# Performance work log

Measured on AMD Instinct MI355X. Metric: run time of the kernel, lower is better.

The kernel has to match this reference:

```python
import jax, jax.numpy as jnp
import numpy as np

B, L, DIM = 4, 2048, 256
NSETS, PP, POSP, LTMP = 4, 4, 16, 16
PI = float(np.pi)


def setup_inputs() -> dict:
    key = jax.random.key(0)
    ks = jax.random.split(key, 8)
    d = DIM
    return {
        "x": jax.random.normal(ks[0], (B, L, d), jnp.float32),
        "key_proj": jax.random.normal(ks[1], (d, NSETS * PP), jnp.float32) / np.sqrt(d),
        "query_proj": jax.random.normal(ks[2], (d, NSETS * PP), jnp.float32) / np.sqrt(d),
        "ltm_key_proj": jax.random.normal(ks[3], (3 * d, LTMP), jnp.float32) / np.sqrt(3 * d),
        "pos_freqs": jnp.exp(jnp.arange(POSP, dtype=jnp.float32) * (-np.log(10000.0) / POSP)),
        "w_value": jax.random.normal(ks[4], (d, d), jnp.float32) / np.sqrt(d),
        "b_value": jnp.zeros(d, jnp.float32),
        "w_ltm_val": jax.random.normal(ks[5], (d, d), jnp.float32) / np.sqrt(d),
        "b_ltm_val": jnp.zeros(d, jnp.float32),
        "ln_gamma": jnp.ones(d, jnp.float32),
        "ln_beta": jnp.zeros(d, jnp.float32),
        "w_out": jax.random.normal(ks[6], (d, d), jnp.float32) / np.sqrt(d),
        "b_out": jnp.zeros(d, jnp.float32),
        "set_weights": jnp.ones(NSETS, jnp.float32),
        "pos_weight": jnp.ones(1, jnp.float32),
        "surprise_scale": jnp.array(5.0, jnp.float32),
        "surprise_bias": jnp.array(0.0, jnp.float32),
        "resonance_scale": jnp.array(5.0, jnp.float32),
        "resonance_threshold": jnp.array(0.3, jnp.float32),
        "ltm_weight": jnp.array(0.5, jnp.float32),
        "ltm_binding_memory": jnp.zeros((LTMP, d), jnp.complex64),
        "ltm_count": jnp.array(0.0, jnp.float32),
    }


def reference(x, key_proj, query_proj, ltm_key_proj, pos_freqs, w_value, b_value,
              w_ltm_val, b_ltm_val, ln_gamma, ln_beta, w_out, b_out, set_weights,
              pos_weight, surprise_scale, surprise_bias, resonance_scale,
              resonance_threshold, ltm_weight, ltm_binding_memory, ltm_count):
    Bx, Lx, D = x.shape
    # phasor encodings
    key_ph = jnp.exp(1j * (jnp.tanh(x @ key_proj) * PI)).reshape(Bx, Lx, NSETS, PP)
    qry_ph = jnp.exp(1j * (jnp.tanh(x @ query_proj) * PI)).reshape(Bx, Lx, NSETS, PP)
    V_real = x @ w_value + b_value
    weights = jax.nn.softmax(set_weights)
    # joint (cross-bank) phasors
    jk = jnp.prod(key_ph, axis=2)   # [B,L,PP]
    jq = jnp.prod(qry_ph, axis=2)
    # exclusive cumsum of joint keys -> resonance-based surprise write gate
    km = jnp.concatenate([jnp.zeros_like(jk[:, :1]), jnp.cumsum(jk[:, :-1], axis=1)], axis=1)
    rmag = jnp.abs(km * jnp.conj(jq)).mean(-1, keepdims=True)
    posf = jnp.maximum(jnp.arange(Lx, dtype=jnp.float32), 1.0)
    nres = rmag / jnp.sqrt(posf)[None, :, None]
    sc = jnp.clip(resonance_scale, 1.0, 20.0)
    th = jnp.clip(resonance_threshold, 0.1, 0.9)
    surprise = 0.5 * (1.0 - jnp.tanh(sc * (nres - th)))
    gate = jax.nn.sigmoid(surprise_scale * (surprise - 0.5) + surprise_bias)
    Vg = (V_real * gate).astype(jnp.complex64)
    # cross-bank holographic memory (joint key binding)
    cross = jnp.real((jnp.cumsum(jk[..., None] * Vg[:, :, None, :], axis=1)
                      * jnp.conj(jq)[..., None]).sum(2))
    # per-bank holographic memory over all planes
    bound_all = key_ph[..., None] * Vg[:, :, None, None, :]            # [B,L,S,P,D]
    mem_all = jnp.cumsum(bound_all.reshape(Bx, Lx, NSETS * PP, D), axis=1)
    mem_all = mem_all.reshape(Bx, Lx, NSETS, PP, D)
    per_bank = jnp.real((mem_all * jnp.conj(qry_ph)[..., None]).sum(3))  # [B,L,S,D]
    total = (per_bank * weights[None, None, :, None]).sum(2)
    total = (total + cross) / (NSETS + 1.0)
    # positional phasor memory (ungated V)
    pos_ph = jnp.exp(1j * (jnp.arange(Lx, dtype=jnp.float32)[:, None] * pos_freqs * 2.0 * PI))  # [L,P]
    Vc = V_real.astype(jnp.complex64)
    ret_pos = jnp.real((jnp.cumsum(pos_ph[None, :, :, None] * Vc[:, :, None, :], axis=1)
                        * jnp.conj(pos_ph)[None, :, :, None]).sum(2))
    total = 0.5 * total + 0.5 * (jax.nn.sigmoid(pos_weight) * ret_pos)  # fixed_gate = 0.5
    # LTM retrieval from persistent binding memory (detached buffers)
    p1 = jnp.arange(1, Lx + 1, dtype=jnp.float32)[None, :, None]
    rm = jnp.cumsum(x, axis=1) / p1
    rv = jnp.cumsum(x * x, axis=1) / p1 - rm * rm
    rs = jnp.sqrt(jnp.clip(rv, 1e-8, None))
    ltm_ph = jnp.exp(1j * (jnp.tanh(jnp.concatenate([x, rm, rs], -1) @ ltm_key_proj) * PI))  # [B,L,LTMP]
    pers = jnp.real((ltm_binding_memory[None, None] * jnp.conj(ltm_ph)[..., None]).sum(2))
    pnorm = jnp.sqrt(jnp.maximum(ltm_count, 1.0) * LTMP)
    total = total + jax.nn.sigmoid(ltm_weight) * (pers / pnorm)
    # output: LayerNorm + Linear on normalized retrieval, residual
    nrm = jnp.sqrt(jnp.arange(1, Lx + 1, dtype=jnp.float32) * PP)[None, :, None]
    h = total / nrm
    mu = h.mean(-1, keepdims=True)
    var = ((h - mu) ** 2).mean(-1, keepdims=True)
    hn = (h - mu) / jnp.sqrt(var + 1e-5) * ln_gamma + ln_beta
    return x + hn @ w_out + b_out
```

## Files before the change

kernel.cpp:

```cpp
#include <hip/hip_runtime.h>
#include <math.h>

#define B 4
#define L 2048
#define D 256
#define POSP 16
#define LTMP 16
#define T 64
#define C 32
#define F 72
#define PI_F 3.14159274101257324f
#define TWO_PI_D 6.283185307179586476925286766559

__global__ __launch_bounds__(256) void prep_kernel(const float* __restrict__ pos_freqs,
                                                   const float* __restrict__ lkp,
                                                   const float* __restrict__ x,
                                                   float* __restrict__ posci,
                                                   float* __restrict__ Wt,
                                                   float* __restrict__ Sx16,
                                                   float* __restrict__ Sxx16) {
    int bid = blockIdx.x;
    int tid = threadIdx.x;
    if (bid < 128) {
        int idx = bid * 256 + tid;
        int t = idx >> 4, p = idx & 15;
        float a = (float)t * pos_freqs[p];
        float th = (a * 2.0f) * PI_F;
        double r = fmod((double)th, TWO_PI_D);
        posci[t * 32 + 2 * p] = (float)cos(r);
        posci[t * 32 + 2 * p + 1] = (float)sin(r);
    } else if (bid < 176) {
        int i2 = (bid - 128) * 256 + tid;
        if (i2 < 16 * 768) {
            int p = i2 / 768, j = i2 - p * 768;
            Wt[i2] = lkp[j * 16 + p];
        }
    } else {
        int sb = bid - 176;
        int s = sb & 127, b = sb >> 7;
        float sx = 0.f, sxx = 0.f;
#pragma unroll
        for (int k = 0; k < 16; k++) {
            float v = x[((size_t)(b * L + s * 16 + k)) * D + tid];
            sx += v; sxx += v * v;
        }
        Sx16[((size_t)(b * 128 + s)) * D + tid] = sx;
        Sxx16[((size_t)(b * 128 + s)) * D + tid] = sxx;
    }
}

__global__ __launch_bounds__(256) void featurize_kernel(
    const float* __restrict__ x, const float* __restrict__ key_proj,
    const float* __restrict__ query_proj, const float* __restrict__ w_value,
    const float* __restrict__ b_value, const float* __restrict__ set_weights,
    float* __restrict__ V, float* __restrict__ fk, float* __restrict__ fq,
    float* __restrict__ partial) {
    int cg = blockIdx.x;
    int rc = blockIdx.y;
    int b  = blockIdx.z;
    int row0 = rc * 64;
    int tid = threadIdx.x;
    __shared__ float xs[2][32][74];
    __shared__ float ws[2][32][84];
    __shared__ float zbuf[64][20];
    __shared__ float jkv[64][9];
    const bool has_proj = (cg < 2);
    const float* proj = (cg == 0) ? key_proj : query_proj;
    int rg = tid >> 4, cgi = tid & 15;
    int r0 = rg * 4, c0 = cgi * 4;
    int prow = tid >> 2, pc4 = tid & 3;
    float acc[4][4], accp[4];
#pragma unroll
    for (int i = 0; i < 4; i++) {
#pragma unroll
        for (int e = 0; e < 4; e++) acc[i][e] = 0.f;
        accp[i] = 0.f;
    }
    int rrA = tid >> 3, k4A = tid & 7;
    int jA = tid >> 4, c4A = tid & 15;
    float4 xr0, xr1, wr0, wr1, prr;

#define ISSUE_LOADS(kb_)                                                            \
    {                                                                               \
        xr0 = *(const float4*)(x + ((size_t)(b * L + row0 + rrA)) * D + (kb_) + k4A * 4);      \
        xr1 = *(const float4*)(x + ((size_t)(b * L + row0 + 32 + rrA)) * D + (kb_) + k4A * 4); \
        wr0 = *(const float4*)(w_value + (size_t)((kb_) + jA) * D + cg * 64 + c4A * 4);        \
        wr1 = *(const float4*)(w_value + (size_t)((kb_) + 16 + jA) * D + cg * 64 + c4A * 4);   \
        if (has_proj && tid < 128)                                                  \
            prr = *(const float4*)(proj + (size_t)((kb_) + (tid >> 2)) * 16 + (tid & 3) * 4);  \
    }
#define WRITE_LDS(bi)                                                               \
    {                                                                               \
        const float* xp0 = (const float*)&xr0;                                      \
        const float* xp1 = (const float*)&xr1;                                      \
        _Pragma("unroll")                                                           \
        for (int u = 0; u < 4; u++) {                                               \
            xs[bi][k4A * 4 + u][rrA] = xp0[u];                                      \
            xs[bi][k4A * 4 + u][32 + rrA] = xp1[u];                                 \
        }                                                                           \
        *(float4*)&ws[bi][jA][c4A * 4] = wr0;                                       \
        *(float4*)&ws[bi][16 + jA][c4A * 4] = wr1;                                  \
        if (has_proj && tid < 128)                                                  \
            *(float4*)&ws[bi][tid >> 2][64 + (tid & 3) * 4] = prr;                  \
    }

    ISSUE_LOADS(0);
    WRITE_LDS(0);
    __syncthreads();
    for (int kc = 0; kc < 8; kc++) {
        if (kc < 7) ISSUE_LOADS((kc + 1) * 32);
        int bi = kc & 1;
#pragma unroll 8
        for (int j = 0; j < 32; j++) {
            float2 xlo = *(float2*)&xs[bi][j][r0];
            float2 xhi = *(float2*)&xs[bi][j][r0 + 2];
            float4 wv = *(float4*)&ws[bi][j][c0];
            acc[0][0] += xlo.x * wv.x; acc[0][1] += xlo.x * wv.y; acc[0][2] += xlo.x * wv.z; acc[0][3] += xlo.x * wv.w;
            acc[1][0] += xlo.y * wv.x; acc[1][1] += xlo.y * wv.y; acc[1][2] += xlo.y * wv.z; acc[1][3] += xlo.y * wv.w;
            acc[2][0] += xhi.x * wv.x; acc[2][1] += xhi.x * wv.y; acc[2][2] += xhi.x * wv.z; acc[2][3] += xhi.x * wv.w;
            acc[3][0] += xhi.y * wv.x; acc[3][1] += xhi.y * wv.y; acc[3][2] += xhi.y * wv.z; acc[3][3] += xhi.y * wv.w;
            if (has_proj) {
                float xp = xs[bi][j][prow];
                float4 wp = *(float4*)&ws[bi][j][64 + pc4 * 4];
                accp[0] += xp * wp.x; accp[1] += xp * wp.y;
                accp[2] += xp * wp.z; accp[3] += xp * wp.w;
            }
        }
        if (kc < 7) WRITE_LDS((kc + 1) & 1);
        __syncthreads();
    }
#undef ISSUE_LOADS
#undef WRITE_LDS

    {
        int d0 = cg * 64 + c0;
        float4 bv = *(const float4*)(b_value + d0);
#pragma unroll
        for (int i = 0; i < 4; i++) {
            size_t o = ((size_t)(b * L + row0 + r0 + i)) * D + d0;
            *(float4*)(V + o) = make_float4(acc[i][0] + bv.x, acc[i][1] + bv.y,
                                            acc[i][2] + bv.z, acc[i][3] + bv.w);
        }
    }
    if (!has_proj) return;
#pragma unroll
    for (int e = 0; e < 4; e++) zbuf[prow][pc4 * 4 + e] = tanhf(accp[e]) * PI_F;
    __syncthreads();
    {
        int tt = tid >> 2, q = tid & 3;
        size_t bt = (size_t)(b * L + row0 + tt);
        if (cg == 0) {
            float* fp = fk + bt * 40;
#pragma unroll
            for (int e = 0; e < 4; e++) {
                int col = q * 4 + e;
                float si, co; sincosf(zbuf[tt][col], &si, &co);
                fp[2 * col] = co; fp[2 * col + 1] = si;
            }
            float zs = zbuf[tt][q] + zbuf[tt][4 + q] + zbuf[tt][8 + q] + zbuf[tt][12 + q];
            float si, co; sincosf(zs, &si, &co);
            fp[32 + 2 * q] = co; fp[33 + 2 * q] = si;
            jkv[tt][2 * q] = co; jkv[tt][2 * q + 1] = si;
        } else {
            float sw0 = set_weights[0], sw1 = set_weights[1], sw2 = set_weights[2], sw3 = set_weights[3];
            float mx = fmaxf(fmaxf(sw0, sw1), fmaxf(sw2, sw3));
            float e0 = expf(sw0 - mx), e1 = expf(sw1 - mx), e2 = expf(sw2 - mx), e3 = expf(sw3 - mx);
            float esum = e0 + e1 + e2 + e3;
            float wsoft[4] = {e0 / esum, e1 / esum, e2 / esum, e3 / esum};
            float* fp = fq + bt * 40;
#pragma unroll
            for (int e = 0; e < 4; e++) {
                int col = q * 4 + e;
                float si, co; sincosf(zbuf[tt][col], &si, &co);
                float sc = 0.1f * wsoft[col >> 2];
                fp[2 * col] = sc * co; fp[2 * col + 1] = sc * si;
            }
            float zs = zbuf[tt][q] + zbuf[tt][4 + q] + zbuf[tt][8 + q] + zbuf[tt][12 + q];
            float si, co; sincosf(zs, &si, &co);
            fp[32 + 2 * q] = 0.1f * co; fp[33 + 2 * q] = 0.1f * si;
        }
    }
    __syncthreads();
    if (cg == 0) {
        int h = tid >> 7, idxr = tid & 127;
        int rr2 = idxr >> 3, ch = idxr & 7;
#pragma unroll
        for (int s2 = 16; s2 >= 1; s2 >>= 1) {
            if (rr2 < s2) jkv[h * 32 + rr2][ch] += jkv[h * 32 + rr2 + s2][ch];
            __syncthreads();
        }
        if (rr2 == 0) partial[((size_t)(b * 64 + rc * 2 + h)) * 8 + ch] = jkv[h * 32][ch];
    }
}

__global__ __launch_bounds__(512) void gs_scan_kernel(const float* __restrict__ partial,
                                                      float* __restrict__ chunkoff) {
    int b = blockIdx.x;
    int tid = threadIdx.x;
    int c = tid >> 3, ch = tid & 7;
    __shared__ float sc_[64][9];
    float own = partial[((size_t)(b * 64 + c)) * 8 + ch];
    sc_[c][ch] = own;
    __syncthreads();
    for (int off = 1; off < 64; off <<= 1) {
        float v = 0.f;
        if (c >= off) v = sc_[c - off][ch];
        __syncthreads();
        if (c >= off) sc_[c][ch] += v;
        __syncthreads();
    }
    chunkoff[((size_t)(b * 64 + c)) * 8 + ch] = sc_[c][ch] - own;
}

__global__ __launch_bounds__(256) void gs_apply_kernel(
    float* __restrict__ fk, const float* __restrict__ chunkoff,
    const float* __restrict__ surprise_scale, const float* __restrict__ surprise_bias,
    const float* __restrict__ resonance_scale, const float* __restrict__ resonance_threshold) {
    int rc = blockIdx.x, b = blockIdx.y;
    int tid = threadIdx.x;
    int t = tid >> 3, ch = tid & 7;
    __shared__ float sc_[32][9];
    __shared__ float gbuf[32];
    float* fp = fk + ((size_t)(b * L + rc * 32 + t)) * 40;
    float own = fp[32 + ch];
    sc_[t][ch] = own;
    __syncthreads();
    for (int off = 1; off < 32; off <<= 1) {
        float v = 0.f;
        if (t >= off) v = sc_[t - off][ch];
        __syncthreads();
        if (t >= off) sc_[t][ch] += v;
        __syncthreads();
    }
    float run = chunkoff[((size_t)(b * 64 + rc)) * 8 + ch] + sc_[t][ch] - own;
    __syncthreads();
    sc_[t][ch] = run;
    __syncthreads();
    if (tid < 32) {
        int tg = rc * 32 + tid;
        float r0 = sc_[tid][0], r1 = sc_[tid][1], r2 = sc_[tid][2], r3 = sc_[tid][3];
        float r4 = sc_[tid][4], r5 = sc_[tid][5], r6 = sc_[tid][6], r7 = sc_[tid][7];
        float rmag = 0.25f * (sqrtf(r0 * r0 + r1 * r1) + sqrtf(r2 * r2 + r3 * r3) +
                              sqrtf(r4 * r4 + r5 * r5) + sqrtf(r6 * r6 + r7 * r7));
        float scv = fminf(fmaxf(resonance_scale[0], 1.f), 20.f);
        float thv = fminf(fmaxf(resonance_threshold[0], 0.1f), 0.9f);
        float nres = rmag / sqrtf(fmaxf((float)tg, 1.0f));
        float surprise = 0.5f * (1.0f - tanhf(scv * (nres - thv)));
        gbuf[tid] = 1.0f / (1.0f + expf(-(surprise_scale[0] * (surprise - 0.5f) + surprise_bias[0])));
    }
    __syncthreads();
    float gv = gbuf[t];
#pragma unroll
    for (int e = 0; e < 5; e++) fp[ch * 5 + e] *= gv;
}

__global__ __launch_bounds__(256) void ltm_z_kernel(
    const float* __restrict__ x, const float* __restrict__ Sx16,
    const float* __restrict__ Sxx16, const float* __restrict__ Wt,
    float* __restrict__ czsz) {
    int s = blockIdx.x, b = blockIdx.y;
    int tid = threadIdx.x;
    __shared__ float xs[16][260], rms[16][260], rss[16][260];
    float a0 = 0.f, a1 = 0.f, a2 = 0.f, a3 = 0.f;
    float c0 = 0.f, c1 = 0.f, c2 = 0.f, c3 = 0.f;
    int sp = 0;
    for (; sp + 4 <= s; sp += 4) {
        a0 += Sx16[((size_t)(b * 128 + sp)) * D + tid];
        a1 += Sx16[((size_t)(b * 128 + sp + 1)) * D + tid];
        a2 += Sx16[((size_t)(b * 128 + sp + 2)) * D + tid];
        a3 += Sx16[((size_t)(b * 128 + sp + 3)) * D + tid];
        c0 += Sxx16[((size_t)(b * 128 + sp)) * D + tid];
        c1 += Sxx16[((size_t)(b * 128 + sp + 1)) * D + tid];
        c2 += Sxx16[((size_t)(b * 128 + sp + 2)) * D + tid];
        c3 += Sxx16[((size_t)(b * 128 + sp + 3)) * D + tid];
    }
    for (; sp < s; sp++) {
        a0 += Sx16[((size_t)(b * 128 + sp)) * D + tid];
        c0 += Sxx16[((size_t)(b * 128 + sp)) * D + tid];
    }
    float runx = (a0 + a1) + (a2 + a3), runxx = (c0 + c1) + (c2 + c3);
    for (int k = 0; k < 16; k++) {
        int tg = s * 16 + k;
        float xv = x[((size_t)(b * L + tg)) * D + tid];
        runx += xv; runxx += xv * xv;
        float n = (float)(tg + 1);
        float rm = runx / n;
        float rv = runxx / n - rm * rm;
        xs[k][tid] = xv; rms[k][tid] = rm;
        rss[k][tid] = sqrtf(fmaxf(rv, 1e-8f));
    }
    __syncthreads();
    int tl = tid & 15, p = tid >> 4;
    const float* W0 = Wt + p * 768;
    float u0 = 0.f, u1 = 0.f, u2 = 0.f;
#pragma unroll 4
    for (int j4 = 0; j4 < 64; j4++) {
        float4 xv = *(float4*)&xs[tl][j4 * 4];
        float4 wx = *(const float4*)(W0 + j4 * 4);
        float4 rv = *(float4*)&rms[tl][j4 * 4];
        float4 wr = *(const float4*)(W0 + 256 + j4 * 4);
        float4 sv = *(float4*)&rss[tl][j4 * 4];
        float4 wz = *(const float4*)(W0 + 512 + j4 * 4);
        u0 += xv.x * wx.x + xv.y * wx.y + xv.z * wx.z + xv.w * wx.w;
        u1 += rv.x * wr.x + rv.y * wr.y + rv.z * wr.z + rv.w * wr.w;
        u2 += sv.x * wz.x + sv.y * wz.y + sv.z * wz.z + sv.w * wz.w;
    }
    float z = tanhf(u0 + u1 + u2) * PI_F;
    float si, co; sincosf(z, &si, &co);
    int tg = s * 16 + tl;
    czsz[((size_t)(b * L + tg)) * 32 + p] = co;
    czsz[((size_t)(b * L + tg)) * 32 + 16 + p] = si;
}

__global__ __launch_bounds__(256) void outer_sums_kernel(
    const float* __restrict__ V, const float* __restrict__ fk,
    const float* __restrict__ posci, float* __restrict__ Sh) {
    int g = blockIdx.x >> 1, h = blockIdx.x & 1;
    int c = blockIdx.y;
    int b = blockIdx.z;
    int tid = threadIdx.x;
    __shared__ float Fk[32][40];
    int F0 = g * 36;
#pragma unroll
    for (int e = 0; e < 2; e++) {
        int idx = e * 256 + tid;
        if (idx < 288) {
            int r = idx / 9, c4 = idx - r * 9;
            int tg = c * T + h * 32 + r;
            float4 v;
            if (g == 0) v = *(const float4*)(fk + ((size_t)(b * L + tg)) * 40 + c4 * 4);
            else if (c4 == 0) v = *(const float4*)(fk + ((size_t)(b * L + tg)) * 40 + 36);
            else v = *(const float4*)(posci + tg * 32 + (c4 - 1) * 4);
            *(float4*)&Fk[r][c4 * 4] = v;
        }
    }
    __syncthreads();
    float acc[36];
#pragma unroll
    for (int f = 0; f < 36; f++) acc[f] = 0.f;
    for (int t = 0; t < 32; t++) {
        float v = V[((size_t)(b * L + c * T + h * 32 + t)) * D + tid];
#pragma unroll
        for (int f4 = 0; f4 < 9; f4++) {
            float4 fkv = *(float4*)&Fk[t][f4 * 4];
            acc[f4 * 4 + 0] += fkv.x * v;
            acc[f4 * 4 + 1] += fkv.y * v;
            acc[f4 * 4 + 2] += fkv.z * v;
            acc[f4 * 4 + 3] += fkv.w * v;
        }
    }
    for (int f = 0; f < 36; f++)
        Sh[((((size_t)(b * C + c)) * 2 + h) * F + F0 + f) * D + tid] = acc[f];
}

__global__ __launch_bounds__(256) void prefix_kernel(const float* __restrict__ Sh,
                                                     float* __restrict__ S) {
    int bf = blockIdx.x;
    int b = bf / F, f = bf % F;
    int d = threadIdx.x;
    float v0[C], v1[C];
#pragma unroll
    for (int c = 0; c < C; c++) {
        v0[c] = Sh[((((size_t)(b * C + c)) * 2 + 0) * F + f) * D + d];
        v1[c] = Sh[((((size_t)(b * C + c)) * 2 + 1) * F + f) * D + d];
    }
    float run = 0.f;
#pragma unroll
    for (int c = 0; c < C; c++) {
        S[(((size_t)(b * C + c)) * F + f) * D + d] = run;
        run += v0[c] + v1[c];
    }
}

__global__ __launch_bounds__(256) void intra_kernel(
    const float* __restrict__ V, float* __restrict__ ret,
    const float* __restrict__ fk, const float* __restrict__ fq,
    const float* __restrict__ posci, const float* __restrict__ Mexc,
    const float* __restrict__ pos_weight) {
    int tg = blockIdx.x >> 1, dh = blockIdx.x & 1;
    int c = blockIdx.y, b = blockIdx.z;
    int tid = threadIdx.x;
    int t0 = tg * 16;
    __shared__ float Fk[64][76];
    __shared__ float Fq[16][76];
    __shared__ float As[16][68];
    float posq = 0.5f / (1.0f + expf(-pos_weight[0]));
#pragma unroll
    for (int e = 0; e < 5; e++) {
        int idx = e * 256 + tid;
        if (idx < 1152) {
            int r = idx / 18, c4 = idx - r * 18;
            int tgl = c * T + r;
            float4 v;
            if (c4 < 10) v = *(const float4*)(fk + ((size_t)(b * L + tgl)) * 40 + c4 * 4);
            else v = *(const float4*)(posci + tgl * 32 + (c4 - 10) * 4);
            *(float4*)&Fk[r][c4 * 4] = v;
        }
    }
#pragma unroll
    for (int e = 0; e < 2; e++) {
        int idx = e * 256 + tid;
        if (idx < 288) {
            int r = idx / 18, c4 = idx - r * 18;
            int tgl = c * T + t0 + r;
            float4 v;
            if (c4 < 10) v = *(const float4*)(fq + ((size_t)(b * L + tgl)) * 40 + c4 * 4);
            else {
                v = *(const float4*)(posci + tgl * 32 + (c4 - 10) * 4);
                v.x *= posq; v.y *= posq; v.z *= posq; v.w *= posq;
            }
            *(float4*)&Fq[r][c4 * 4] = v;
        }
    }
    __syncthreads();
    {
        int r = tid >> 4, k0 = (tid & 15) * 4;
        int tglob = t0 + r;
        float a0 = 0.f, a1 = 0.f, a2 = 0.f, a3 = 0.f;
#pragma unroll
        for (int f4 = 0; f4 < 18; f4++) {
            float4 q = *(float4*)&Fq[r][f4 * 4];
            float4 k0v = *(float4*)&Fk[k0 + 0][f4 * 4];
            float4 k1v = *(float4*)&Fk[k0 + 1][f4 * 4];
            float4 k2v = *(float4*)&Fk[k0 + 2][f4 * 4];
            float4 k3v = *(float4*)&Fk[k0 + 3][f4 * 4];
            a0 += q.x * k0v.x + q.y * k0v.y + q.z * k0v.z + q.w * k0v.w;
            a1 += q.x * k1v.x + q.y * k1v.y + q.z * k1v.z + q.w * k1v.w;
            a2 += q.x * k2v.x + q.y * k2v.y + q.z * k2v.z + q.w * k2v.w;
            a3 += q.x * k3v.x + q.y * k3v.y + q.z * k3v.z + q.w * k3v.w;
        }
        float4 av = make_float4((k0 + 0 <= tglob) ? a0 : 0.f, (k0 + 1 <= tglob) ? a1 : 0.f,
                                (k0 + 2 <= tglob) ? a2 : 0.f, (k0 + 3 <= tglob) ? a3 : 0.f);
        *(float4*)&As[tid >> 4][k0] = av;
    }
    __syncthreads();
    int dl = tid & 127, rowg = tid >> 7;
    int d = dh * 128 + dl;
    int r0 = rowg * 8;
    float acc[8];
#pragma unroll
    for (int i = 0; i < 8; i++) acc[i] = 0.f;
    const float* Mp = Mexc + (((size_t)(b * C + c)) * F) * D + d;
#pragma unroll 8
    for (int f = 0; f < F; f++) {
        float m = Mp[(size_t)f * D];
#pragma unroll
        for (int i = 0; i < 8; i++) acc[i] += Fq[r0 + i][f] * m;
    }
    const float* Vp = V + ((size_t)(b * L + c * T)) * D + d;
    int kmax = t0 + 16;
#pragma unroll 8
    for (int k = 0; k < kmax; k++) {
        float v = Vp[(size_t)k * D];
#pragma unroll
        for (int i = 0; i < 8; i++) acc[i] += As[r0 + i][k] * v;
    }
    float* Rp = ret + ((size_t)(b * L + c * T + t0 + r0)) * D + d;
#pragma unroll
    for (int i = 0; i < 8; i++) Rp[(size_t)i * D] = acc[i];
}

__global__ __launch_bounds__(256) void hprep_kernel(
    const float* __restrict__ retp, const float* __restrict__ czsz,
    const float* __restrict__ ltm_mem, const float* __restrict__ ltm_count,
    const float* __restrict__ ltm_weight, const float* __restrict__ ln_gamma,
    const float* __restrict__ ln_beta, float* __restrict__ hn) {
    int rc = blockIdx.x;
    int b  = blockIdx.y;
    int row0 = rc * 16;
    int tid = threadIdx.x;
    __shared__ float hb[16][260];
    __shared__ float cs[16][33];
    __shared__ float part1[16][17], part2[16][17];
    __shared__ float mu[16], rsig[16];
    float lsig = 1.f / (1.f + expf(-ltm_weight[0]));
    float pnorm = sqrtf(fmaxf(ltm_count[0], 1.f) * (float)LTMP);
    float lcoef = lsig / pnorm;
    float Mre[16], Mim[16];
#pragma unroll
    for (int p = 0; p < 16; p++) {
        Mre[p] = ltm_mem[(p * D + tid) * 2];
        Mim[p] = ltm_mem[(p * D + tid) * 2 + 1];
    }
    float gam = ln_gamma[tid], bet = ln_beta[tid];
#pragma unroll
    for (int e = 0; e < 2; e++) {
        int idx = e * 256 + tid;
        int t = idx >> 5, q = idx & 31;
        cs[t][q] = czsz[((size_t)(b * L + row0 + t)) * 32 + q];
    }
    __syncthreads();
#pragma unroll 4
    for (int t = 0; t < 16; t++) {
        int tg = row0 + t;
        float pers = 0.f;
#pragma unroll
        for (int p = 0; p < 16; p++) pers += Mre[p] * cs[t][p] + Mim[p] * cs[t][16 + p];
        float rv = retp[((size_t)(b * L + tg)) * D + tid];
        hb[t][tid] = (rv + lcoef * pers) / (2.0f * sqrtf((float)(tg + 1)));
    }
    __syncthreads();
    {
        int row = tid & 15, e = tid >> 4;
        float s1 = 0.f, s2 = 0.f;
#pragma unroll
        for (int k = 0; k < 16; k++) {
            float v = hb[row][e + 16 * k];
            s1 += v; s2 += v * v;
        }
        part1[row][e] = s1; part2[row][e] = s2;
    }
    __syncthreads();
    if (tid < 16) {
        float s1 = 0.f, s2 = 0.f;
#pragma unroll
        for (int e = 0; e < 16; e++) { s1 += part1[tid][e]; s2 += part2[tid][e]; }
        float m = s1 / 256.f;
        mu[tid] = m;
        rsig[tid] = rsqrtf(fmaxf(s2 / 256.f - m * m, 0.f) + 1e-5f);
    }
    __syncthreads();
#pragma unroll 4
    for (int t = 0; t < 16; t++)
        hn[((size_t)(b * L + row0 + t)) * D + tid] =
            (hb[t][tid] - mu[t]) * rsig[t] * gam + bet;
}

__global__ __launch_bounds__(256) void gemm_out_kernel(
    const float* __restrict__ hn, const float* __restrict__ w_out,
    const float* __restrict__ b_out, const float* __restrict__ x,
    float* __restrict__ out) {
    int cg = blockIdx.x;
    int rc = blockIdx.y;
    int b  = blockIdx.z;
    int row0 = rc * 64;
    int tid = threadIdx.x;
    __shared__ float hs[2][32][74];
    __shared__ float wo[2][32][68];
    int rg = tid >> 4, cgi = tid & 15;
    int r0 = rg * 4, c0 = cgi * 4;
    float acc[4][4];
#pragma unroll
    for (int i = 0; i < 4; i++)
#pragma unroll
        for (int e = 0; e < 4; e++) acc[i][e] = 0.f;
    int rrA = tid >> 3, k4A = tid & 7;
    int jA = tid >> 4, c4A = tid & 15;
    float4 hr0, hr1, wr0, wr1;

#define ISSUE_LOADS(kb_)                                                            \
    {                                                                               \
        hr0 = *(const float4*)(hn + ((size_t)(b * L + row0 + rrA)) * D + (kb_) + k4A * 4);      \
        hr1 = *(const float4*)(hn + ((size_t)(b * L + row0 + 32 + rrA)) * D + (kb_) + k4A * 4); \
        wr0 = *(const float4*)(w_out + (size_t)((kb_) + jA) * D + cg * 64 + c4A * 4);           \
        wr1 = *(const float4*)(w_out + (size_t)((kb_) + 16 + jA) * D + cg * 64 + c4A * 4);      \
    }
#define WRITE_LDS(bi)                                                               \
    {                                                                               \
        const float* hp0 = (const float*)&hr0;                                      \
        const float* hp1 = (const float*)&hr1;                                      \
        _Pragma("unroll")                                                           \
        for (int u = 0; u < 4; u++) {                                               \
            hs[bi][k4A * 4 + u][rrA] = hp0[u];                                      \
            hs[bi][k4A * 4 + u][32 + rrA] = hp1[u];                                 \
        }                                                                           \
        *(float4*)&wo[bi][jA][c4A * 4] = wr0;                                       \
        *(float4*)&wo[bi][16 + jA][c4A * 4] = wr1;                                  \
    }

    ISSUE_LOADS(0);
    WRITE_LDS(0);
    __syncthreads();
    for (int kc = 0; kc < 8; kc++) {
        if (kc < 7) ISSUE_LOADS((kc + 1) * 32);
        int bi = kc & 1;
#pragma unroll 8
        for (int j = 0; j < 32; j++) {
            float2 xlo = *(float2*)&hs[bi][j][r0];
            float2 xhi = *(float2*)&hs[bi][j][r0 + 2];
            float4 wv = *(float4*)&wo[bi][j][c0];
            acc[0][0] += xlo.x * wv.x; acc[0][1] += xlo.x * wv.y; acc[0][2] += xlo.x * wv.z; acc[0][3] += xlo.x * wv.w;
            acc[1][0] += xlo.y * wv.x; acc[1][1] += xlo.y * wv.y; acc[1][2] += xlo.y * wv.z; acc[1][3] += xlo.y * wv.w;
            acc[2][0] += xhi.x * wv.x; acc[2][1] += xhi.x * wv.y; acc[2][2] += xhi.x * wv.z; acc[2][3] += xhi.x * wv.w;
            acc[3][0] += xhi.y * wv.x; acc[3][1] += xhi.y * wv.y; acc[3][2] += xhi.y * wv.z; acc[3][3] += xhi.y * wv.w;
        }
        if (kc < 7) WRITE_LDS((kc + 1) & 1);
        __syncthreads();
    }
#undef ISSUE_LOADS
#undef WRITE_LDS
    {
        int d0 = cg * 64 + c0;
        float4 bo = *(const float4*)(b_out + d0);
#pragma unroll
        for (int i = 0; i < 4; i++) {
            size_t o = ((size_t)(b * L + row0 + r0 + i)) * D + d0;
            float4 xa = *(const float4*)(x + o);
            *(float4*)(out + o) = make_float4(xa.x + acc[i][0] + bo.x, xa.y + acc[i][1] + bo.y,
                                              xa.z + acc[i][2] + bo.z, xa.w + acc[i][3] + bo.w);
        }
    }
}

extern "C" void kernel_launch(void* const* d_in, const int* in_sizes, int n_in,
                              void* d_out, int out_size, void* d_ws, size_t ws_size,
                              hipStream_t stream) {
    (void)in_sizes; (void)n_in; (void)out_size; (void)ws_size;
    const float* x            = (const float*)d_in[0];
    const float* key_proj     = (const float*)d_in[1];
    const float* query_proj   = (const float*)d_in[2];
    const float* ltm_key_proj = (const float*)d_in[3];
    const float* pos_freqs    = (const float*)d_in[4];
    const float* w_value      = (const float*)d_in[5];
    const float* b_value      = (const float*)d_in[6];
    const float* ln_gamma     = (const float*)d_in[9];
    const float* ln_beta      = (const float*)d_in[10];
    const float* w_out        = (const float*)d_in[11];
    const float* b_out        = (const float*)d_in[12];
    const float* set_weights  = (const float*)d_in[13];
    const float* pos_weight   = (const float*)d_in[14];
    const float* surprise_scale      = (const float*)d_in[15];
    const float* surprise_bias       = (const float*)d_in[16];
    const float* resonance_scale     = (const float*)d_in[17];
    const float* resonance_threshold = (const float*)d_in[18];
    const float* ltm_weight   = (const float*)d_in[19];
    const float* ltm_mem      = (const float*)d_in[20];
    const float* ltm_count    = (const float*)d_in[21];
    float* out = (float*)d_out;

    float* ws = (float*)d_ws;
    size_t off = 0;
    float* V     = ws + off; off += (size_t)B * L * D;
    float* ret   = ws + off; off += (size_t)B * L * D;
    float* fk    = ws + off; off += (size_t)B * L * 40;
    float* fq    = ws + off; off += (size_t)B * L * 40;
    float* posci = ws + off; off += (size_t)L * 32;
    float* Sx16  = ws + off; off += (size_t)B * 128 * D;
    float* Sxx16 = ws + off; off += (size_t)B * 128 * D;
    float* czsz  = ws + off; off += (size_t)B * L * 32;
    float* Sh    = ws + off; off += (size_t)B * C * 2 * F * D;
    float* S     = ws + off; off += (size_t)B * C * F * D;
    float* Wt    = ws + off; off += (size_t)16 * 768;
    float* partial  = ws + off; off += (size_t)B * 64 * 8;
    float* chunkoff = ws + off; off += (size_t)B * 64 * 8;
    float* hn = V;

    prep_kernel<<<dim3(688), 256, 0, stream>>>(pos_freqs, ltm_key_proj, x, posci, Wt,
                                               Sx16, Sxx16);
    featurize_kernel<<<dim3(4, 32, B), 256, 0, stream>>>(x, key_proj, query_proj, w_value,
                                                         b_value, set_weights, V, fk, fq, partial);
    gs_scan_kernel<<<dim3(B), 512, 0, stream>>>(partial, chunkoff);
    gs_apply_kernel<<<dim3(64, B), 256, 0, stream>>>(fk, chunkoff, surprise_scale, surprise_bias,
                                                     resonance_scale, resonance_threshold);
    ltm_z_kernel<<<dim3(128, B), 256, 0, stream>>>(x, Sx16, Sxx16, Wt, czsz);
    outer_sums_kernel<<<dim3(4, C, B), 256, 0, stream>>>(V, fk, posci, Sh);
    prefix_kernel<<<dim3(B * F), 256, 0, stream>>>(Sh, S);
    intra_kernel<<<dim3(8, C, B), 256, 0, stream>>>(V, ret, fk, fq, posci, S, pos_weight);
    hprep_kernel<<<dim3(128, B), 256, 0, stream>>>(ret, czsz, ltm_mem, ltm_count, ltm_weight,
                                                   ln_gamma, ln_beta, hn);
    gemm_out_kernel<<<dim3(4, 32, B), 256, 0, stream>>>(hn, w_out, b_out, x, out);
}
```

Measured before the change: 246.2 us.

## Fuse LTM retrieval and LayerNorm into intra-chunk kernel with 512-thread blocks

Merges hprep_kernel into intra_kernel. Each 512-thread block now covers all 256 feature columns for 16 rows, so the LTM persistent term, the position normalisation and the LayerNorm statistics are computed in-kernel. This removes the global write and re-read of the intermediate ret buffer and one kernel launch. It also trims the causal V loop per half-block (kmax = t0+r0+8) and halves the grid, which may reduce the number of blocks available for occupancy.

```diff
diff --git a/kernel.cpp b/kernel.cpp
--- a/kernel.cpp
+++ b/kernel.cpp
@@ -372,22 +372,31 @@
     }
 }
 
-__global__ __launch_bounds__(256) void intra_kernel(
-    const float* __restrict__ V, float* __restrict__ ret,
+__global__ __launch_bounds__(512) void intra_kernel(
+    const float* __restrict__ V, float* __restrict__ hn,
     const float* __restrict__ fk, const float* __restrict__ fq,
     const float* __restrict__ posci, const float* __restrict__ Mexc,
-    const float* __restrict__ pos_weight) {
-    int tg = blockIdx.x >> 1, dh = blockIdx.x & 1;
-    int c = blockIdx.y, b = blockIdx.z;
+    const float* __restrict__ pos_weight, const float* __restrict__ czsz,
+    const float* __restrict__ ltm_mem, const float* __restrict__ ltm_count,
+    const float* __restrict__ ltm_weight, const float* __restrict__ ln_gamma,
+    const float* __restrict__ ln_beta) {
+    int tg = blockIdx.x, c = blockIdx.y, b = blockIdx.z;
     int tid = threadIdx.x;
     int t0 = tg * 16;
-    __shared__ float Fk[64][76];
-    __shared__ float Fq[16][76];
-    __shared__ float As[16][68];
+    __shared__ float smem[8384];
+    float (*Fk)[76] = (float(*)[76])smem;
+    float (*Fq)[76] = (float(*)[76])(smem + 4864);
+    float (*As)[68] = (float(*)[68])(smem + 6080);
+    float (*cs)[33]  = (float(*)[33])(smem + 7168);
+    float (*part1)[17] = (float(*)[17])(smem + 7696);
+    float (*part2)[17] = (float(*)[17])(smem + 7968);
+    float* mu   = smem + 8240;
+    float* rsig = smem + 8256;
+    float (*hb)[260] = (float(*)[260])smem;
     float posq = 0.5f / (1.0f + expf(-pos_weight[0]));
 #pragma unroll
-    for (int e = 0; e < 5; e++) {
-        int idx = e * 256 + tid;
+    for (int e = 0; e < 3; e++) {
+        int idx = e * 512 + tid;
         if (idx < 1152) {
             int r = idx / 18, c4 = idx - r * 18;
             int tgl = c * T + r;
@@ -397,46 +406,40 @@
             *(float4*)&Fk[r][c4 * 4] = v;
         }
     }
-#pragma unroll
-    for (int e = 0; e < 2; e++) {
-        int idx = e * 256 + tid;
-        if (idx < 288) {
-            int r = idx / 18, c4 = idx - r * 18;
-            int tgl = c * T + t0 + r;
-            float4 v;
-            if (c4 < 10) v = *(const float4*)(fq + ((size_t)(b * L + tgl)) * 40 + c4 * 4);
-            else {
-                v = *(const float4*)(posci + tgl * 32 + (c4 - 10) * 4);
-                v.x *= posq; v.y *= posq; v.z *= posq; v.w *= posq;
-            }
-            *(float4*)&Fq[r][c4 * 4] = v;
-        }
-    }
-    __syncthreads();
+    if (tid < 288) {
+        int r = tid / 18, c4 = tid - r * 18;
+        int tgl = c * T + t0 + r;
+        float4 v;
+        if (c4 < 10) v = *(const float4*)(fq + ((size_t)(b * L + tgl)) * 40 + c4 * 4);
+        else {
+            v = *(const float4*)(posci + tgl * 32 + (c4 - 10) * 4);
+            v.x *= posq; v.y *= posq; v.z *= posq; v.w *= posq;
+        }
+        *(float4*)&Fq[r][c4 * 4] = v;
+    }
     {
-        int r = tid >> 4, k0 = (tid & 15) * 4;
+        int t = tid >> 5, q = tid & 31;
+        cs[t][q] = czsz[((size_t)(b * L + c * T + t0 + t)) * 32 + q];
+    }
+    __syncthreads();
+    {
+        int r = tid >> 5, kA = tid & 31;
         int tglob = t0 + r;
-        float a0 = 0.f, a1 = 0.f, a2 = 0.f, a3 = 0.f;
+        float a0 = 0.f, a1 = 0.f;
 #pragma unroll
         for (int f4 = 0; f4 < 18; f4++) {
             float4 q = *(float4*)&Fq[r][f4 * 4];
-            float4 k0v = *(float4*)&Fk[k0 + 0][f4 * 4];
-            float4 k1v = *(float4*)&Fk[k0 + 1][f4 * 4];
-            float4 k2v = *(float4*)&Fk[k0 + 2][f4 * 4];
-            float4 k3v = *(float4*)&Fk[k0 + 3][f4 * 4];
-            a0 += q.x * k0v.x + q.y * k0v.y + q.z * k0v.z + q.w * k0v.w;
-            a1 += q.x * k1v.x + q.y * k1v.y + q.z * k1v.z + q.w * k1v.w;
-            a2 += q.x * k2v.x + q.y * k2v.y + q.z * k2v.z + q.w * k2v.w;
-            a3 += q.x * k3v.x + q.y * k3v.y + q.z * k3v.z + q.w * k3v.w;
-        }
-        float4 av = make_float4((k0 + 0 <= tglob) ? a0 : 0.f, (k0 + 1 <= tglob) ? a1 : 0.f,
-                                (k0 + 2 <= tglob) ? a2 : 0.f, (k0 + 3 <= tglob) ? a3 : 0.f);
-        *(float4*)&As[tid >> 4][k0] = av;
-    }
-    __syncthreads();
-    int dl = tid & 127, rowg = tid >> 7;
-    int d = dh * 128 + dl;
-    int r0 = rowg * 8;
+            float4 kv0 = *(float4*)&Fk[kA][f4 * 4];
+            float4 kv1 = *(float4*)&Fk[kA + 32][f4 * 4];
+            a0 += q.x * kv0.x + q.y * kv0.y + q.z * kv0.z + q.w * kv0.w;
+            a1 += q.x * kv1.x + q.y * kv1.y + q.z * kv1.z + q.w * kv1.w;
+        }
+        As[r][kA] = (kA <= tglob) ? a0 : 0.f;
+        As[r][kA + 32] = (kA + 32 <= tglob) ? a1 : 0.f;
+    }
+    __syncthreads();
+    int d = tid & 255, half = tid >> 8;
+    int r0 = half * 8;
     float acc[8];
 #pragma unroll
     for (int i = 0; i < 8; i++) acc[i] = 0.f;
@@ -448,59 +451,36 @@
         for (int i = 0; i < 8; i++) acc[i] += Fq[r0 + i][f] * m;
     }
     const float* Vp = V + ((size_t)(b * L + c * T)) * D + d;
-    int kmax = t0 + 16;
+    int kmax = t0 + r0 + 8;
 #pragma unroll 8
     for (int k = 0; k < kmax; k++) {
         float v = Vp[(size_t)k * D];
 #pragma unroll
         for (int i = 0; i < 8; i++) acc[i] += As[r0 + i][k] * v;
     }
-    float* Rp = ret + ((size_t)(b * L + c * T + t0 + r0)) * D + d;
-#pragma unroll
-    for (int i = 0; i < 8; i++) Rp[(size_t)i * D] = acc[i];
-}
-
-__global__ __launch_bounds__(256) void hprep_kernel(
-    const float* __restrict__ retp, const float* __restrict__ czsz,
-    const float* __restrict__ ltm_mem, const float* __restrict__ ltm_count,
-    const float* __restrict__ ltm_weight, const float* __restrict__ ln_gamma,
-    const float* __restrict__ ln_beta, float* __restrict__ hn) {
-    int rc = blockIdx.x;
-    int b  = blockIdx.y;
-    int row0 = rc * 16;
-    int tid = threadIdx.x;
-    __shared__ float hb[16][260];
-    __shared__ float cs[16][33];
-    __shared__ float part1[16][17], part2[16][17];
-    __shared__ float mu[16], rsig[16];
     float lsig = 1.f / (1.f + expf(-ltm_weight[0]));
     float pnorm = sqrtf(fmaxf(ltm_count[0], 1.f) * (float)LTMP);
     float lcoef = lsig / pnorm;
     float Mre[16], Mim[16];
 #pragma unroll
     for (int p = 0; p < 16; p++) {
-        Mre[p] = ltm_mem[(p * D + tid) * 2];
-        Mim[p] = ltm_mem[(p * D + tid) * 2 + 1];
-    }
-    float gam = ln_gamma[tid], bet = ln_beta[tid];
-#pragma unroll
-    for (int e = 0; e < 2; e++) {
-        int idx = e * 256 + tid;
-        int t = idx >> 5, q = idx & 31;
-        cs[t][q] = czsz[((size_t)(b * L + row0 + t)) * 32 + q];
-    }
-    __syncthreads();
-#pragma unroll 4
-    for (int t = 0; t < 16; t++) {
-        int tg = row0 + t;
+        Mre[p] = ltm_mem[(p * D + d) * 2];
+        Mim[p] = ltm_mem[(p * D + d) * 2 + 1];
+    }
+#pragma unroll
+    for (int i = 0; i < 8; i++) {
+        int row = r0 + i;
         float pers = 0.f;
 #pragma unroll
-        for (int p = 0; p < 16; p++) pers += Mre[p] * cs[t][p] + Mim[p] * cs[t][16 + p];
-        float rv = retp[((size_t)(b * L + tg)) * D + tid];
-        hb[t][tid] = (rv + lcoef * pers) / (2.0f * sqrtf((float)(tg + 1)));
-    }
-    __syncthreads();
-    {
+        for (int p = 0; p < 16; p++) pers += Mre[p] * cs[row][p] + Mim[p] * cs[row][16 + p];
+        int tgl = c * T + t0 + row;
+        acc[i] = (acc[i] + lcoef * pers) / (2.0f * sqrtf((float)(tgl + 1)));
+    }
+    __syncthreads();
+#pragma unroll
+    for (int i = 0; i < 8; i++) hb[r0 + i][d] = acc[i];
+    __syncthreads();
+    if (tid < 256) {
         int row = tid & 15, e = tid >> 4;
         float s1 = 0.f, s2 = 0.f;
 #pragma unroll
@@ -520,10 +500,13 @@
         rsig[tid] = rsqrtf(fmaxf(s2 / 256.f - m * m, 0.f) + 1e-5f);
     }
     __syncthreads();
-#pragma unroll 4
-    for (int t = 0; t < 16; t++)
-        hn[((size_t)(b * L + row0 + t)) * D + tid] =
-            (hb[t][tid] - mu[t]) * rsig[t] * gam + bet;
+    float gam = ln_gamma[d], bet = ln_beta[d];
+#pragma unroll
+    for (int i = 0; i < 8; i++) {
+        int row = r0 + i;
+        hn[((size_t)(b * L + c * T + t0 + row)) * D + d] =
+            (acc[i] - mu[row]) * rsig[row] * gam + bet;
+    }
 }
 
 __global__ __launch_bounds__(256) void gemm_out_kernel(
@@ -631,7 +614,7 @@
     float* ws = (float*)d_ws;
     size_t off = 0;
     float* V     = ws + off; off += (size_t)B * L * D;
-    float* ret   = ws + off; off += (size_t)B * L * D;
+    float* hn    = ws + off; off += (size_t)B * L * D;
     float* fk    = ws + off; off += (size_t)B * L * 40;
     float* fq    = ws + off; off += (size_t)B * L * 40;
     float* posci = ws + off; off += (size_t)L * 32;
@@ -643,7 +626,6 @@
     float* Wt    = ws + off; off += (size_t)16 * 768;
     float* partial  = ws + off; off += (size_t)B * 64 * 8;
     float* chunkoff = ws + off; off += (size_t)B * 64 * 8;
-    float* hn = V;
 
     prep_kernel<<<dim3(688), 256, 0, stream>>>(pos_freqs, ltm_key_proj, x, posci, Wt,
                                                Sx16, Sxx16);
@@ -655,8 +637,8 @@
     ltm_z_kernel<<<dim3(128, B), 256, 0, stream>>>(x, Sx16, Sxx16, Wt, czsz);
     outer_sums_kernel<<<dim3(4, C, B), 256, 0, stream>>>(V, fk, posci, Sh);
     prefix_kernel<<<dim3(B * F), 256, 0, stream>>>(Sh, S);
-    intra_kernel<<<dim3(8, C, B), 256, 0, stream>>>(V, ret, fk, fq, posci, S, pos_weight);
-    hprep_kernel<<<dim3(128, B), 256, 0, stream>>>(ret, czsz, ltm_mem, ltm_count, ltm_weight,
-                                                   ln_gamma, ln_beta, hn);
+    intra_kernel<<<dim3(4, C, B), 512, 0, stream>>>(V, hn, fk, fq, posci, S, pos_weight,
+                                                    czsz, ltm_mem, ltm_count, ltm_weight,
+                                                    ln_gamma, ln_beta);
     gemm_out_kernel<<<dim3(4, 32, B), 256, 0, stream>>>(hn, w_out, b_out, x, out);
 }
```

Result: faster. 221.5 us (-10.0%).
